# Kernel optimization log

Measured on AMD Instinct MI355X. Metric: run time of the kernel, lower is better.

The kernel has to match this reference:

```python
import jax, jax.numpy as jnp
import numpy as np

H = 50  # hidden_size hardcoded in the module


def _rnn_layer(x, w_ih, w_hh, b_ih, b_hh):
    # x: [B, T, F]; PyTorch nn.RNN (tanh): h_t = tanh(x_t W_ih^T + b_ih + h_{t-1} W_hh^T + b_hh)
    B = x.shape[0]
    # precompute input projection for all timesteps: [B, T, H]
    xp = jnp.einsum('btf,hf->bth', x, w_ih) + b_ih + b_hh
    h0 = jnp.zeros((B, H), dtype=x.dtype)

    def step(h, xp_t):
        h_new = jnp.tanh(xp_t + h @ w_hh.T)
        return h_new, h_new

    _, hs = jax.lax.scan(step, h0, jnp.swapaxes(xp, 0, 1))  # hs: [T, B, H]
    return jnp.swapaxes(hs, 0, 1)  # [B, T, H]


def setup_inputs() -> dict:
    key = jax.random.key(0)
    ks = jax.random.split(key, 12)
    B, T, F = 8192, 256, 64
    s_in = 1.0 / np.sqrt(H)
    u = lambda k, shape: jax.random.uniform(k, shape, jnp.float32, -s_in, s_in)
    return {
        'x': jax.random.normal(ks[0], (B, T, F), jnp.float32),
        'w_ih1': u(ks[1], (H, F)),
        'w_hh1': u(ks[2], (H, H)),
        'b_ih1': u(ks[3], (H,)),
        'b_hh1': u(ks[4], (H,)),
        'w_ih2': u(ks[5], (H, H)),
        'w_hh2': u(ks[6], (H, H)),
        'b_ih2': u(ks[7], (H,)),
        'b_hh2': u(ks[8], (H,)),
        'fc_w': u(ks[9], (1, H)),
        'fc_b': u(ks[10], (1,)),
    }


def reference(x, w_ih1, w_hh1, b_ih1, b_hh1, w_ih2, w_hh2, b_ih2, b_hh2, fc_w, fc_b):
    h1 = _rnn_layer(x, w_ih1, w_hh1, b_ih1, b_hh1)   # [B, T, H]
    h2 = _rnn_layer(h1, w_ih2, w_hh2, b_ih2, b_hh2)  # [B, T, H]
    last = jax.nn.relu(h2[:, -1, :])                  # [B, H]
    return jax.nn.sigmoid(last @ fc_w.T + fc_b)       # [B, 1]
```

## Files before the change

kernel.cpp:

```cpp
#include <hip/hip_runtime.h>


#define BATCH   8192
#define TSTEPS  256
#define FIN     64
#define HID     50
#define ROWS    16
#define ST      72
#define PFD     4

typedef _Float16 f16x8 __attribute__((ext_vector_type(8)));
typedef _Float16 f16x4 __attribute__((ext_vector_type(4)));
typedef float    f32x4 __attribute__((ext_vector_type(4)));

#define LGKM0() asm volatile("s_waitcnt lgkmcnt(0)" ::: "memory")

__device__ __forceinline__ float tanh_fast(float v) {
    float e = __builtin_amdgcn_exp2f(v * 2.8853900817779268f);
    return 1.0f - 2.0f * __builtin_amdgcn_rcpf(e + 1.0f);
}

__global__ __launch_bounds__(64, 1)
void rnn_fused(const float* __restrict__ x,
               const float* __restrict__ w_ih1, const float* __restrict__ w_hh1,
               const float* __restrict__ b_ih1, const float* __restrict__ b_hh1,
               const float* __restrict__ w_ih2, const float* __restrict__ w_hh2,
               const float* __restrict__ b_ih2, const float* __restrict__ b_hh2,
               const float* __restrict__ fc_w,  const float* __restrict__ fc_b,
               float* __restrict__ out)
{
    __shared__ __align__(16) _Float16 lds_h1[ROWS * ST];
    __shared__ __align__(16) _Float16 lds_h2[ROWS * ST];

    const int lane = threadIdx.x & 63;
    const int c    = lane & 15;
    const int q    = lane >> 4;
    const int rowbase = blockIdx.x * ROWS;

    f16x8 Wih1[4][2], Whh1[4][2], Wih2[4][2], Whh2[4][2];
#pragma unroll
    for (int jt = 0; jt < 4; ++jt) {
        const int j = jt * 16 + c;
#pragma unroll
        for (int kc = 0; kc < 2; ++kc) {
            f16x8 a, b, g, d;
#pragma unroll
            for (int i = 0; i < 8; ++i) {
                const int k = kc * 32 + q * 8 + i;
                a[i] = (_Float16)((j < HID)            ? w_ih1[j * FIN + k] : 0.0f);
                b[i] = (_Float16)((j < HID && k < HID) ? w_hh1[j * HID + k] : 0.0f);
                g[i] = (_Float16)((j < HID && k < HID) ? w_ih2[j * HID + k] : 0.0f);
                d[i] = (_Float16)((j < HID && k < HID) ? w_hh2[j * HID + k] : 0.0f);
            }
            Wih1[jt][kc] = a; Whh1[jt][kc] = b; Wih2[jt][kc] = g; Whh2[jt][kc] = d;
        }
    }

    f32x4 b1v[4], b2v[4], fcv[4];
#pragma unroll
    for (int jt = 0; jt < 4; ++jt) {
#pragma unroll
        for (int r = 0; r < 4; ++r) {
            const int j = jt * 16 + q * 4 + r;
            b1v[jt][r] = (j < HID) ? b_ih1[j] + b_hh1[j] : 0.0f;
            b2v[jt][r] = (j < HID) ? b_ih2[j] + b_hh2[j] : 0.0f;
            fcv[jt][r] = (j < HID) ? fc_w[j] : 0.0f;
        }
    }
    const float fcb = fc_b[0];

    const float* xrow = x + (size_t)(rowbase + c) * TSTEPS * FIN + q * 8;
    f32x4 xf[PFD][4];
#pragma unroll
    for (int p = 0; p < PFD; ++p) {
        const float* src = xrow + (size_t)p * FIN;
        xf[p][0] = *(const f32x4*)(src);
        xf[p][1] = *(const f32x4*)(src + 4);
        xf[p][2] = *(const f32x4*)(src + 32);
        xf[p][3] = *(const f32x4*)(src + 36);
    }

    f16x8 h1b[2] = {}, h2b[2] = {};
    f32x4 h2f[4] = {};

    for (int t0 = 0; t0 < TSTEPS; t0 += PFD) {
#pragma unroll
        for (int u = 0; u < PFD; ++u) {
            const int t = t0 + u;

            f16x8 xb0, xb1;
#pragma unroll
            for (int i = 0; i < 4; ++i) {
                xb0[i]     = (_Float16)xf[u][0][i];
                xb0[4 + i] = (_Float16)xf[u][1][i];
                xb1[i]     = (_Float16)xf[u][2][i];
                xb1[4 + i] = (_Float16)xf[u][3][i];
            }
            {
                const int tn = (t + PFD < TSTEPS) ? t + PFD : TSTEPS - 1;
                const float* src = xrow + (size_t)tn * FIN;
                xf[u][0] = *(const f32x4*)(src);
                xf[u][1] = *(const f32x4*)(src + 4);
                xf[u][2] = *(const f32x4*)(src + 32);
                xf[u][3] = *(const f32x4*)(src + 36);
            }

            f32x4 a1[4];
#pragma unroll
            for (int jt = 0; jt < 4; ++jt) {
                f32x4 a = b1v[jt];
                a = __builtin_amdgcn_mfma_f32_16x16x32_f16(Wih1[jt][0], xb0,    a, 0, 0, 0);
                a = __builtin_amdgcn_mfma_f32_16x16x32_f16(Wih1[jt][1], xb1,    a, 0, 0, 0);
                a = __builtin_amdgcn_mfma_f32_16x16x32_f16(Whh1[jt][0], h1b[0], a, 0, 0, 0);
                a = __builtin_amdgcn_mfma_f32_16x16x32_f16(Whh1[jt][1], h1b[1], a, 0, 0, 0);
                a1[jt] = a;
            }
#pragma unroll
            for (int jt = 0; jt < 4; ++jt) {
                f16x4 v;
#pragma unroll
                for (int r = 0; r < 4; ++r) {
                    const float tv = (jt < 3 || r < 2) ? tanh_fast(a1[jt][r]) : a1[jt][r];
                    v[r] = (_Float16)tv;
                }
                *(f16x4*)&lds_h1[c * ST + jt * 16 + q * 4] = v;
            }
            LGKM0();
            h1b[0] = *(const f16x8*)&lds_h1[c * ST + q * 8];
            h1b[1] = *(const f16x8*)&lds_h1[c * ST + 32 + q * 8];

            f32x4 a2[4];
#pragma unroll
            for (int jt = 0; jt < 4; ++jt) {
                f32x4 a = b2v[jt];
                a = __builtin_amdgcn_mfma_f32_16x16x32_f16(Whh2[jt][0], h2b[0], a, 0, 0, 0);
                a = __builtin_amdgcn_mfma_f32_16x16x32_f16(Whh2[jt][1], h2b[1], a, 0, 0, 0);
                a2[jt] = a;
            }
#pragma unroll
            for (int jt = 0; jt < 4; ++jt) {
                f32x4 a = a2[jt];
                a = __builtin_amdgcn_mfma_f32_16x16x32_f16(Wih2[jt][0], h1b[0], a, 0, 0, 0);
                a = __builtin_amdgcn_mfma_f32_16x16x32_f16(Wih2[jt][1], h1b[1], a, 0, 0, 0);
                a2[jt] = a;
            }
#pragma unroll
            for (int jt = 0; jt < 4; ++jt) {
                f16x4 v;
#pragma unroll
                for (int r = 0; r < 4; ++r) {
                    const float tv = (jt < 3 || r < 2) ? tanh_fast(a2[jt][r]) : a2[jt][r];
                    h2f[jt][r] = tv;
                    v[r] = (_Float16)tv;
                }
                *(f16x4*)&lds_h2[c * ST + jt * 16 + q * 4] = v;
            }
            LGKM0();
            h2b[0] = *(const f16x8*)&lds_h2[c * ST + q * 8];
            h2b[1] = *(const f16x8*)&lds_h2[c * ST + 32 + q * 8];
        }
    }

    float s = 0.0f;
#pragma unroll
    for (int jt = 0; jt < 4; ++jt)
#pragma unroll
        for (int r = 0; r < 4; ++r) {
            const float h = h2f[jt][r];
            s += fcv[jt][r] * (h > 0.0f ? h : 0.0f);
        }
    s += __shfl_xor(s, 16, 64);
    s += __shfl_xor(s, 32, 64);
    if (lane < 16) {
        const float z = s + fcb;
        const float e = __builtin_amdgcn_exp2f(-z * 1.4426950408889634f);
        out[rowbase + lane] = __builtin_amdgcn_rcpf(1.0f + e);
    }
}

extern "C" void kernel_launch(void* const* d_in, const int* in_sizes, int n_in,
                              void* d_out, int out_size, void* d_ws, size_t ws_size,
                              hipStream_t stream) {
    (void)in_sizes; (void)n_in; (void)out_size; (void)d_ws; (void)ws_size;
    const float* x     = (const float*)d_in[0];
    const float* w_ih1 = (const float*)d_in[1];
    const float* w_hh1 = (const float*)d_in[2];
    const float* b_ih1 = (const float*)d_in[3];
    const float* b_hh1 = (const float*)d_in[4];
    const float* w_ih2 = (const float*)d_in[5];
    const float* w_hh2 = (const float*)d_in[6];
    const float* b_ih2 = (const float*)d_in[7];
    const float* b_hh2 = (const float*)d_in[8];
    const float* fc_w  = (const float*)d_in[9];
    const float* fc_b  = (const float*)d_in[10];
    float* out = (float*)d_out;

    rnn_fused<<<dim3(BATCH / ROWS), dim3(64), 0, stream>>>(
        x, w_ih1, w_hh1, b_ih1, b_hh1, w_ih2, w_hh2, b_ih2, b_hh2, fc_w, fc_b, out);
}
```

Measured before the change: 772.5 us.

## Split RNN stages across four wavefronts as a barrier-synchronized pipeline

Replaces the single-wavefront per-block kernel with four specialized wavefronts. They compute, in order, the layer-1 input projection, the layer-1 recurrence, the layer-2 input projection and the layer-2 recurrence, each skewed by one timestep. Values pass between them through double-buffered LDS, with a workgroup barrier every step. The tanh scale is also folded into the weights and biases so the activation skips a multiply. The aim is to overlap the independent projection work with the serial recurrences, at the cost of 256+ barriers per block and a longer per-step critical path through LDS.

```diff
diff --git a/kernel.cpp b/kernel.cpp
--- a/kernel.cpp
+++ b/kernel.cpp
@@ -7,20 +7,22 @@
 #define HID     50
 #define ROWS    16
 #define ST      72
-#define PFD     4
+#define NITER   260
+#define SCALE   2.8853900817779268f
 
 typedef _Float16 f16x8 __attribute__((ext_vector_type(8)));
 typedef _Float16 f16x4 __attribute__((ext_vector_type(4)));
 typedef float    f32x4 __attribute__((ext_vector_type(4)));
 
+#define BAR()   asm volatile("s_waitcnt lgkmcnt(0)\n\ts_barrier" ::: "memory")
 #define LGKM0() asm volatile("s_waitcnt lgkmcnt(0)" ::: "memory")
 
-__device__ __forceinline__ float tanh_fast(float v) {
-    float e = __builtin_amdgcn_exp2f(v * 2.8853900817779268f);
+__device__ __forceinline__ float tanh_pre(float v) {
+    float e = __builtin_amdgcn_exp2f(v);
     return 1.0f - 2.0f * __builtin_amdgcn_rcpf(e + 1.0f);
 }
 
-__global__ __launch_bounds__(64, 1)
+__global__ __launch_bounds__(256, 2)
 void rnn_fused(const float* __restrict__ x,
                const float* __restrict__ w_ih1, const float* __restrict__ w_hh1,
                const float* __restrict__ b_ih1, const float* __restrict__ b_hh1,
@@ -29,152 +31,258 @@
                const float* __restrict__ fc_w,  const float* __restrict__ fc_b,
                float* __restrict__ out)
 {
-    __shared__ __align__(16) _Float16 lds_h1[ROWS * ST];
+    __shared__ __align__(16) float    lds_xp[2][4][4][16][4];
+    __shared__ __align__(16) float    lds_p2[2][4][4][16][4];
+    __shared__ __align__(16) _Float16 lds_h1[2][ROWS * ST];
     __shared__ __align__(16) _Float16 lds_h2[ROWS * ST];
 
-    const int lane = threadIdx.x & 63;
+    const int tid  = threadIdx.x;
+    const int wid  = tid >> 6;
+    const int lane = tid & 63;
     const int c    = lane & 15;
     const int q    = lane >> 4;
     const int rowbase = blockIdx.x * ROWS;
 
-    f16x8 Wih1[4][2], Whh1[4][2], Wih2[4][2], Whh2[4][2];
-#pragma unroll
-    for (int jt = 0; jt < 4; ++jt) {
-        const int j = jt * 16 + c;
-#pragma unroll
-        for (int kc = 0; kc < 2; ++kc) {
-            f16x8 a, b, g, d;
-#pragma unroll
-            for (int i = 0; i < 8; ++i) {
-                const int k = kc * 32 + q * 8 + i;
-                a[i] = (_Float16)((j < HID)            ? w_ih1[j * FIN + k] : 0.0f);
-                b[i] = (_Float16)((j < HID && k < HID) ? w_hh1[j * HID + k] : 0.0f);
-                g[i] = (_Float16)((j < HID && k < HID) ? w_ih2[j * HID + k] : 0.0f);
-                d[i] = (_Float16)((j < HID && k < HID) ? w_hh2[j * HID + k] : 0.0f);
-            }
-            Wih1[jt][kc] = a; Whh1[jt][kc] = b; Wih2[jt][kc] = g; Whh2[jt][kc] = d;
-        }
-    }
-
-    f32x4 b1v[4], b2v[4], fcv[4];
-#pragma unroll
-    for (int jt = 0; jt < 4; ++jt) {
-#pragma unroll
-        for (int r = 0; r < 4; ++r) {
-            const int j = jt * 16 + q * 4 + r;
-            b1v[jt][r] = (j < HID) ? b_ih1[j] + b_hh1[j] : 0.0f;
-            b2v[jt][r] = (j < HID) ? b_ih2[j] + b_hh2[j] : 0.0f;
-            fcv[jt][r] = (j < HID) ? fc_w[j] : 0.0f;
-        }
-    }
-    const float fcb = fc_b[0];
-
-    const float* xrow = x + (size_t)(rowbase + c) * TSTEPS * FIN + q * 8;
-    f32x4 xf[PFD][4];
-#pragma unroll
-    for (int p = 0; p < PFD; ++p) {
-        const float* src = xrow + (size_t)p * FIN;
-        xf[p][0] = *(const f32x4*)(src);
-        xf[p][1] = *(const f32x4*)(src + 4);
-        xf[p][2] = *(const f32x4*)(src + 32);
-        xf[p][3] = *(const f32x4*)(src + 36);
-    }
-
-    f16x8 h1b[2] = {}, h2b[2] = {};
-    f32x4 h2f[4] = {};
-
-    for (int t0 = 0; t0 < TSTEPS; t0 += PFD) {
-#pragma unroll
-        for (int u = 0; u < PFD; ++u) {
-            const int t = t0 + u;
-
-            f16x8 xb0, xb1;
-#pragma unroll
-            for (int i = 0; i < 4; ++i) {
-                xb0[i]     = (_Float16)xf[u][0][i];
-                xb0[4 + i] = (_Float16)xf[u][1][i];
-                xb1[i]     = (_Float16)xf[u][2][i];
-                xb1[4 + i] = (_Float16)xf[u][3][i];
-            }
-            {
-                const int tn = (t + PFD < TSTEPS) ? t + PFD : TSTEPS - 1;
-                const float* src = xrow + (size_t)tn * FIN;
-                xf[u][0] = *(const f32x4*)(src);
-                xf[u][1] = *(const f32x4*)(src + 4);
-                xf[u][2] = *(const f32x4*)(src + 32);
-                xf[u][3] = *(const f32x4*)(src + 36);
-            }
-
-            f32x4 a1[4];
-#pragma unroll
-            for (int jt = 0; jt < 4; ++jt) {
-                f32x4 a = b1v[jt];
-                a = __builtin_amdgcn_mfma_f32_16x16x32_f16(Wih1[jt][0], xb0,    a, 0, 0, 0);
-                a = __builtin_amdgcn_mfma_f32_16x16x32_f16(Wih1[jt][1], xb1,    a, 0, 0, 0);
-                a = __builtin_amdgcn_mfma_f32_16x16x32_f16(Whh1[jt][0], h1b[0], a, 0, 0, 0);
-                a = __builtin_amdgcn_mfma_f32_16x16x32_f16(Whh1[jt][1], h1b[1], a, 0, 0, 0);
-                a1[jt] = a;
-            }
-#pragma unroll
-            for (int jt = 0; jt < 4; ++jt) {
-                f16x4 v;
-#pragma unroll
-                for (int r = 0; r < 4; ++r) {
-                    const float tv = (jt < 3 || r < 2) ? tanh_fast(a1[jt][r]) : a1[jt][r];
-                    v[r] = (_Float16)tv;
-                }
-                *(f16x4*)&lds_h1[c * ST + jt * 16 + q * 4] = v;
-            }
-            LGKM0();
-            h1b[0] = *(const f16x8*)&lds_h1[c * ST + q * 8];
-            h1b[1] = *(const f16x8*)&lds_h1[c * ST + 32 + q * 8];
-
-            f32x4 a2[4];
-#pragma unroll
-            for (int jt = 0; jt < 4; ++jt) {
-                f32x4 a = b2v[jt];
-                a = __builtin_amdgcn_mfma_f32_16x16x32_f16(Whh2[jt][0], h2b[0], a, 0, 0, 0);
-                a = __builtin_amdgcn_mfma_f32_16x16x32_f16(Whh2[jt][1], h2b[1], a, 0, 0, 0);
-                a2[jt] = a;
-            }
-#pragma unroll
-            for (int jt = 0; jt < 4; ++jt) {
-                f32x4 a = a2[jt];
-                a = __builtin_amdgcn_mfma_f32_16x16x32_f16(Wih2[jt][0], h1b[0], a, 0, 0, 0);
-                a = __builtin_amdgcn_mfma_f32_16x16x32_f16(Wih2[jt][1], h1b[1], a, 0, 0, 0);
-                a2[jt] = a;
-            }
-#pragma unroll
-            for (int jt = 0; jt < 4; ++jt) {
-                f16x4 v;
-#pragma unroll
-                for (int r = 0; r < 4; ++r) {
-                    const float tv = (jt < 3 || r < 2) ? tanh_fast(a2[jt][r]) : a2[jt][r];
-                    h2f[jt][r] = tv;
-                    v[r] = (_Float16)tv;
-                }
-                *(f16x4*)&lds_h2[c * ST + jt * 16 + q * 4] = v;
-            }
-            LGKM0();
-            h2b[0] = *(const f16x8*)&lds_h2[c * ST + q * 8];
-            h2b[1] = *(const f16x8*)&lds_h2[c * ST + 32 + q * 8];
-        }
-    }
-
-    float s = 0.0f;
-#pragma unroll
-    for (int jt = 0; jt < 4; ++jt)
-#pragma unroll
-        for (int r = 0; r < 4; ++r) {
-            const float h = h2f[jt][r];
-            s += fcv[jt][r] * (h > 0.0f ? h : 0.0f);
-        }
-    s += __shfl_xor(s, 16, 64);
-    s += __shfl_xor(s, 32, 64);
-    if (lane < 16) {
-        const float z = s + fcb;
-        const float e = __builtin_amdgcn_exp2f(-z * 1.4426950408889634f);
-        out[rowbase + lane] = __builtin_amdgcn_rcpf(1.0f + e);
+    if (wid == 0) {
+        f16x8 W[4][2];
+#pragma unroll
+        for (int jt = 0; jt < 4; ++jt) {
+            const int j = jt * 16 + c;
+#pragma unroll
+            for (int kc = 0; kc < 2; ++kc) {
+                f16x8 a;
+#pragma unroll
+                for (int i = 0; i < 8; ++i) {
+                    const int k = kc * 32 + q * 8 + i;
+                    a[i] = (_Float16)((j < HID) ? w_ih1[j * FIN + k] * SCALE : 0.0f);
+                }
+                W[jt][kc] = a;
+            }
+        }
+        f32x4 bv[4];
+#pragma unroll
+        for (int jt = 0; jt < 4; ++jt)
+#pragma unroll
+            for (int r = 0; r < 4; ++r) {
+                const int j = jt * 16 + q * 4 + r;
+                bv[jt][r] = (j < HID) ? (b_ih1[j] + b_hh1[j]) * SCALE : 0.0f;
+            }
+
+        const float* xrow = x + (size_t)(rowbase + c) * TSTEPS * FIN + q * 8;
+        f32x4 xf[4][4];
+#pragma unroll
+        for (int p = 0; p < 4; ++p) {
+            const float* src = xrow + (size_t)p * FIN;
+            xf[p][0] = *(const f32x4*)(src);
+            xf[p][1] = *(const f32x4*)(src + 4);
+            xf[p][2] = *(const f32x4*)(src + 32);
+            xf[p][3] = *(const f32x4*)(src + 36);
+        }
+
+        for (int i0 = 0; i0 < NITER; i0 += 4) {
+#pragma unroll
+            for (int u = 0; u < 4; ++u) {
+                const int i = i0 + u;
+                if (i < TSTEPS) {
+                    f16x8 xb0, xb1;
+#pragma unroll
+                    for (int e = 0; e < 4; ++e) {
+                        xb0[e]     = (_Float16)xf[u][0][e];
+                        xb0[4 + e] = (_Float16)xf[u][1][e];
+                        xb1[e]     = (_Float16)xf[u][2][e];
+                        xb1[4 + e] = (_Float16)xf[u][3][e];
+                    }
+                    {
+                        const int tn = (i + 4 < TSTEPS) ? i + 4 : TSTEPS - 1;
+                        const float* src = xrow + (size_t)tn * FIN;
+                        xf[u][0] = *(const f32x4*)(src);
+                        xf[u][1] = *(const f32x4*)(src + 4);
+                        xf[u][2] = *(const f32x4*)(src + 32);
+                        xf[u][3] = *(const f32x4*)(src + 36);
+                    }
+#pragma unroll
+                    for (int jt = 0; jt < 4; ++jt) {
+                        f32x4 a = bv[jt];
+                        a = __builtin_amdgcn_mfma_f32_16x16x32_f16(W[jt][0], xb0, a, 0, 0, 0);
+                        a = __builtin_amdgcn_mfma_f32_16x16x32_f16(W[jt][1], xb1, a, 0, 0, 0);
+                        *(f32x4*)&lds_xp[u & 1][jt][q][c][0] = a;
+                    }
+                }
+                BAR();
+            }
+        }
+    } else if (wid == 1) {
+        f16x8 W[4][2];
+#pragma unroll
+        for (int jt = 0; jt < 4; ++jt) {
+            const int j = jt * 16 + c;
+#pragma unroll
+            for (int kc = 0; kc < 2; ++kc) {
+                f16x8 a;
+#pragma unroll
+                for (int i = 0; i < 8; ++i) {
+                    const int k = kc * 32 + q * 8 + i;
+                    a[i] = (_Float16)((j < HID && k < HID) ? w_hh1[j * HID + k] * SCALE : 0.0f);
+                }
+                W[jt][kc] = a;
+            }
+        }
+        f16x8 hb[2] = {};
+
+        for (int i0 = 0; i0 < NITER; i0 += 4) {
+#pragma unroll
+            for (int u = 0; u < 4; ++u) {
+                const int i = i0 + u;
+                if (i >= 1 && i <= TSTEPS) {
+                    const int par = (u + 1) & 1;
+                    f32x4 a[4];
+#pragma unroll
+                    for (int jt = 0; jt < 4; ++jt)
+                        a[jt] = *(const f32x4*)&lds_xp[par][jt][q][c][0];
+#pragma unroll
+                    for (int jt = 0; jt < 4; ++jt) {
+                        a[jt] = __builtin_amdgcn_mfma_f32_16x16x32_f16(W[jt][0], hb[0], a[jt], 0, 0, 0);
+                        a[jt] = __builtin_amdgcn_mfma_f32_16x16x32_f16(W[jt][1], hb[1], a[jt], 0, 0, 0);
+                    }
+#pragma unroll
+                    for (int jt = 0; jt < 4; ++jt) {
+                        f16x4 v;
+#pragma unroll
+                        for (int r = 0; r < 4; ++r) {
+                            const float tv = (jt < 3 || r < 2) ? tanh_pre(a[jt][r]) : a[jt][r];
+                            v[r] = (_Float16)tv;
+                        }
+                        *(f16x4*)&lds_h1[par][c * ST + jt * 16 + q * 4] = v;
+                    }
+                    LGKM0();
+                    hb[0] = *(const f16x8*)&lds_h1[par][c * ST + q * 8];
+                    hb[1] = *(const f16x8*)&lds_h1[par][c * ST + 32 + q * 8];
+                }
+                BAR();
+            }
+        }
+    } else if (wid == 2) {
+        f16x8 W[4][2];
+#pragma unroll
+        for (int jt = 0; jt < 4; ++jt) {
+            const int j = jt * 16 + c;
+#pragma unroll
+            for (int kc = 0; kc < 2; ++kc) {
+                f16x8 a;
+#pragma unroll
+                for (int i = 0; i < 8; ++i) {
+                    const int k = kc * 32 + q * 8 + i;
+                    a[i] = (_Float16)((j < HID && k < HID) ? w_ih2[j * HID + k] * SCALE : 0.0f);
+                }
+                W[jt][kc] = a;
+            }
+        }
+        f32x4 bv[4];
+#pragma unroll
+        for (int jt = 0; jt < 4; ++jt)
+#pragma unroll
+            for (int r = 0; r < 4; ++r) {
+                const int j = jt * 16 + q * 4 + r;
+                bv[jt][r] = (j < HID) ? (b_ih2[j] + b_hh2[j]) * SCALE : 0.0f;
+            }
+
+        for (int i0 = 0; i0 < NITER; i0 += 4) {
+#pragma unroll
+            for (int u = 0; u < 4; ++u) {
+                const int i = i0 + u;
+                if (i >= 2 && i <= TSTEPS + 1) {
+                    const int par = u & 1;
+                    f16x8 hb0 = *(const f16x8*)&lds_h1[par][c * ST + q * 8];
+                    f16x8 hb1 = *(const f16x8*)&lds_h1[par][c * ST + 32 + q * 8];
+#pragma unroll
+                    for (int jt = 0; jt < 4; ++jt) {
+                        f32x4 a = bv[jt];
+                        a = __builtin_amdgcn_mfma_f32_16x16x32_f16(W[jt][0], hb0, a, 0, 0, 0);
+                        a = __builtin_amdgcn_mfma_f32_16x16x32_f16(W[jt][1], hb1, a, 0, 0, 0);
+                        *(f32x4*)&lds_p2[par][jt][q][c][0] = a;
+                    }
+                }
+                BAR();
+            }
+        }
+    } else {
+        f16x8 W[4][2];
+#pragma unroll
+        for (int jt = 0; jt < 4; ++jt) {
+            const int j = jt * 16 + c;
+#pragma unroll
+            for (int kc = 0; kc < 2; ++kc) {
+                f16x8 a;
+#pragma unroll
+                for (int i = 0; i < 8; ++i) {
+                    const int k = kc * 32 + q * 8 + i;
+                    a[i] = (_Float16)((j < HID && k < HID) ? w_hh2[j * HID + k] * SCALE : 0.0f);
+                }
+                W[jt][kc] = a;
+            }
+        }
+        f32x4 fcv[4];
+#pragma unroll
+        for (int jt = 0; jt < 4; ++jt)
+#pragma unroll
+            for (int r = 0; r < 4; ++r) {
+                const int j = jt * 16 + q * 4 + r;
+                fcv[jt][r] = (j < HID) ? fc_w[j] : 0.0f;
+            }
+        const float fcb = fc_b[0];
+
+        f16x8 hb[2] = {};
+        f32x4 h2f[4] = {};
+
+        for (int i0 = 0; i0 < NITER; i0 += 4) {
+#pragma unroll
+            for (int u = 0; u < 4; ++u) {
+                const int i = i0 + u;
+                if (i >= 3 && i <= TSTEPS + 2) {
+                    const int par = (u + 1) & 1;
+                    f32x4 a[4];
+#pragma unroll
+                    for (int jt = 0; jt < 4; ++jt)
+                        a[jt] = *(const f32x4*)&lds_p2[par][jt][q][c][0];
+#pragma unroll
+                    for (int jt = 0; jt < 4; ++jt) {
+                        a[jt] = __builtin_amdgcn_mfma_f32_16x16x32_f16(W[jt][0], hb[0], a[jt], 0, 0, 0);
+                        a[jt] = __builtin_amdgcn_mfma_f32_16x16x32_f16(W[jt][1], hb[1], a[jt], 0, 0, 0);
+                    }
+#pragma unroll
+                    for (int jt = 0; jt < 4; ++jt) {
+                        f16x4 v;
+#pragma unroll
+                        for (int r = 0; r < 4; ++r) {
+                            const float tv = (jt < 3 || r < 2) ? tanh_pre(a[jt][r]) : a[jt][r];
+                            h2f[jt][r] = tv;
+                            v[r] = (_Float16)tv;
+                        }
+                        *(f16x4*)&lds_h2[c * ST + jt * 16 + q * 4] = v;
+                    }
+                    LGKM0();
+                    hb[0] = *(const f16x8*)&lds_h2[c * ST + q * 8];
+                    hb[1] = *(const f16x8*)&lds_h2[c * ST + 32 + q * 8];
+                }
+                BAR();
+            }
+        }
+
+        float s = 0.0f;
+#pragma unroll
+        for (int jt = 0; jt < 4; ++jt)
+#pragma unroll
+            for (int r = 0; r < 4; ++r) {
+                const float h = h2f[jt][r];
+                s += fcv[jt][r] * (h > 0.0f ? h : 0.0f);
+            }
+        s += __shfl_xor(s, 16, 64);
+        s += __shfl_xor(s, 32, 64);
+        if (lane < 16) {
+            const float z = s + fcb;
+            const float e = __builtin_amdgcn_exp2f(-z * 1.4426950408889634f);
+            out[rowbase + lane] = __builtin_amdgcn_rcpf(1.0f + e);
+        }
     }
 }
 
@@ -195,6 +303,6 @@
     const float* fc_b  = (const float*)d_in[10];
     float* out = (float*)d_out;
 
-    rnn_fused<<<dim3(BATCH / ROWS), dim3(64), 0, stream>>>(
+    rnn_fused<<<dim3(BATCH / ROWS), dim3(256), 0, stream>>>(
         x, w_ih1, w_hh1, b_ih1, b_hh1, w_ih2, w_hh2, b_ih2, b_hh2, fc_w, fc_b, out);
 }
```

After: 760.0 us. No clear change (-1.6%).
